# Optimization experiments

Measured on AMD Instinct MI355X. Metric: run time of the kernel, lower is better.

## Reference

```python
import jax, jax.numpy as jnp
import numpy as np

NP = 14      # patches per side
PS = 16      # patch size
L = 12       # transformer blocks
H = 12       # heads
DH = 64      # head dim
D = 768      # hidden dim
S = NP * NP + 1  # 197 tokens
EPS = 1e-5   # torch LayerNorm default eps


def _pos_embed():
    # pos[i, j] = sin(i / 10000^(2*(j//2)/D)) for even j, cos(...) for odd j
    i = jnp.arange(S, dtype=jnp.float32)[:, None]
    j = jnp.arange(D)
    angle = i / jnp.power(jnp.float32(10000.0), (2.0 * (j // 2).astype(jnp.float32)) / D)
    return jnp.where(j % 2 == 0, jnp.sin(angle), jnp.cos(angle))  # [S, D]


def _ln(x, g, b):
    m = jnp.mean(x, axis=-1, keepdims=True)
    v = jnp.mean((x - m) ** 2, axis=-1, keepdims=True)
    return (x - m) / jnp.sqrt(v + EPS) * g + b


def setup_inputs() -> dict:
    key = jax.random.key(0)
    ks = iter(jax.random.split(key, 16))
    r = lambda shape, s=0.02: jax.random.normal(next(ks), shape, dtype=jnp.float32) * s
    return {
        'image': jax.random.normal(next(ks), (32, 3, 224, 224), dtype=jnp.float32),
        'W_embed': r((D, 3 * PS * PS)),
        'b_embed': jnp.zeros((D,), jnp.float32),
        'cls': r((1, D), 1.0),
        'Wq': r((L, H, DH, DH)), 'bq': jnp.zeros((L, H, DH), jnp.float32),
        'Wk': r((L, H, DH, DH)), 'bk': jnp.zeros((L, H, DH), jnp.float32),
        'Wv': r((L, H, DH, DH)), 'bv': jnp.zeros((L, H, DH), jnp.float32),
        'ln1_g': jnp.ones((L, D), jnp.float32), 'ln1_b': jnp.zeros((L, D), jnp.float32),
        'ln2_g': jnp.ones((L, D), jnp.float32), 'ln2_b': jnp.zeros((L, D), jnp.float32),
        'W1': r((L, 4 * D, D)), 'b1': jnp.zeros((L, 4 * D), jnp.float32),
        'W2': r((L, D, 4 * D)), 'b2': jnp.zeros((L, D), jnp.float32),
        'Wh': r((1000, D)), 'bh': jnp.zeros((1000,), jnp.float32),
    }


def reference(image, W_embed, b_embed, cls, Wq, bq, Wk, bk, Wv, bv,
              ln1_g, ln1_b, ln2_g, ln2_b, W1, b1, W2, b2, Wh, bh):
    B = image.shape[0]
    # patchify: (B,C,H,W) -> (B, NP*NP, C*PS*PS), token order row-major over (i,j), flatten order (C,ps,ps)
    patches = image.reshape(B, 3, NP, PS, NP, PS).transpose(0, 2, 4, 1, 3, 5).reshape(B, NP * NP, 3 * PS * PS)
    tokens = patches @ W_embed.T + b_embed                      # [B, 196, D]
    tokens = jnp.concatenate([jnp.broadcast_to(cls[None], (B, 1, D)), tokens], axis=1)  # [B, S, D]
    x = tokens + _pos_embed()[None]
    scale = 1.0 / jnp.sqrt(jnp.float32(DH))
    for l in range(L):
        h = _ln(x, ln1_g[l], ln1_b[l]).reshape(B, S, H, DH)
        q = jnp.einsum('bshd,hed->bshe', h, Wq[l]) + bq[l]
        k = jnp.einsum('bshd,hed->bshe', h, Wk[l]) + bk[l]
        v = jnp.einsum('bshd,hed->bshe', h, Wv[l]) + bv[l]
        att = jax.nn.softmax(jnp.einsum('bshe,bthe->bhst', q, k) * scale, axis=-1)
        o = jnp.einsum('bhst,bthe->bshe', att, v).reshape(B, S, D)
        x = x + o
        h2 = _ln(x, ln2_g[l], ln2_b[l])
        m = jax.nn.gelu(h2 @ W1[l].T + b1[l], approximate=False)  # torch nn.GELU = exact erf
        x = x + m @ W2[l].T + b2[l]
    return x[:, 0] @ Wh.T + bh  # [B, 1000]
```

## Files before the change

### kernel.cpp

```cpp
#include <hip/hip_runtime.h>
#include <math.h>

#define BB 32
#define SS 197
#define DD 768
#define HH 12
#define DHD 64
#define LL 12
#define FF 3072
#define NPATCH 196
#define NTOK (BB * SS)
#define MPAD 6400
#define LNEPS 1e-5f

typedef short bf8_t __attribute__((ext_vector_type(8)));
typedef float f4_t  __attribute__((ext_vector_type(4)));
typedef unsigned short u16x8 __attribute__((ext_vector_type(8)));

__device__ __forceinline__ unsigned short f2bf(float x) {
    unsigned u = __float_as_uint(x);
    return (unsigned short)((u + 0x8000u) >> 16);
}
__device__ __forceinline__ float bf_lo(unsigned u) { return __uint_as_float(u << 16); }

__device__ __forceinline__ void gl_lds16(const void* g, void* l) {
    __builtin_amdgcn_global_load_lds((const __attribute__((address_space(1))) unsigned int*)g,
                                     (__attribute__((address_space(3))) unsigned int*)l, 16, 0, 0);
}

__global__ __launch_bounds__(256) void k_conv(const float* __restrict__ a,
                                              unsigned short* __restrict__ o, int n4) {
    for (int i = blockIdx.x * 256 + threadIdx.x; i < n4; i += gridDim.x * 256) {
        float4 v = ((const float4*)a)[i];
        ushort4 r;
        r.x = f2bf(v.x); r.y = f2bf(v.y); r.z = f2bf(v.z); r.w = f2bf(v.w);
        ((ushort4*)o)[i] = r;
    }
}

__global__ __launch_bounds__(256) void k_patchify(const float* __restrict__ img,
                                                  unsigned short* __restrict__ P) {
    const int total = BB * NPATCH * DD;
    for (int idx = blockIdx.x * 256 + threadIdx.x; idx < total; idx += gridDim.x * 256) {
        int e = idx % DD;
        int rest = idx / DD;
        int p = rest % NPATCH;
        int b = rest / NPATCH;
        int c = e >> 8;
        int pi = (e >> 4) & 15;
        int pj = e & 15;
        int i = p / 14, j = p % 14;
        P[idx] = f2bf(img[(((size_t)b * 3 + c) * 224 + (i * 16 + pi)) * 224 + (j * 16 + pj)]);
    }
}

template <int EPI>
__global__ __launch_bounds__(256) void k_gemm_bf(const unsigned short* __restrict__ A,
                                                 const unsigned short* __restrict__ Bw,
                                                 const float* __restrict__ bias,
                                                 void* __restrict__ Cout,
                                                 int M, int N, int K) {
    __shared__ unsigned short As[128 * 32];
    __shared__ unsigned short Bs[128 * 32];
    const int tid = threadIdx.x;
    const int wave = tid >> 6, lane = tid & 63;
    const int m0 = blockIdx.y << 7, n0 = blockIdx.x << 7;

    const int r0 = tid >> 2, kp = (tid & 3) * 8;
    const unsigned short* gA0 = A + (size_t)(m0 + r0) * K + kp;
    const unsigned short* gA1 = A + (size_t)(m0 + 64 + r0) * K + kp;
    const unsigned short* gB0 = Bw + (size_t)(n0 + r0) * K + kp;
    const unsigned short* gB1 = Bw + (size_t)(n0 + 64 + r0) * K + kp;
    unsigned short* lA0 = &As[tid * 8];
    unsigned short* lA1 = &As[(tid + 256) * 8];
    unsigned short* lB0 = &Bs[tid * 8];
    unsigned short* lB1 = &Bs[(tid + 256) * 8];

    const int mh = (wave >> 1) << 6, nh = (wave & 1) << 6;
    const int lm = lane & 15, kq = lane >> 4;

    f4_t acc[4][4];
#pragma unroll
    for (int i = 0; i < 4; ++i)
#pragma unroll
        for (int j = 0; j < 4; ++j) acc[i][j] = (f4_t){0.f, 0.f, 0.f, 0.f};

    for (int k0 = 0; k0 < K; k0 += 32) {
        gl_lds16(gA0, lA0);
        gl_lds16(gA1, lA1);
        gl_lds16(gB0, lB0);
        gl_lds16(gB1, lB1);
        gA0 += 32; gA1 += 32; gB0 += 32; gB1 += 32;
        __syncthreads();
        bf8_t af[4], bfr[4];
#pragma unroll
        for (int mt = 0; mt < 4; ++mt)
            af[mt] = *(const bf8_t*)&As[(mh + mt * 16 + lm) * 32 + kq * 8];
#pragma unroll
        for (int nt = 0; nt < 4; ++nt)
            bfr[nt] = *(const bf8_t*)&Bs[(nh + nt * 16 + lm) * 32 + kq * 8];
#pragma unroll
        for (int mt = 0; mt < 4; ++mt)
#pragma unroll
            for (int nt = 0; nt < 4; ++nt)
                acc[mt][nt] = __builtin_amdgcn_mfma_f32_16x16x32_bf16(af[mt], bfr[nt],
                                                                      acc[mt][nt], 0, 0, 0);
        __syncthreads();
    }

    const int rbase = m0 + mh + kq * 4;
    const int cbase = n0 + nh + lm;
#pragma unroll
    for (int mt = 0; mt < 4; ++mt) {
#pragma unroll
        for (int nt = 0; nt < 4; ++nt) {
            const int col = cbase + nt * 16;
            const float bv = bias[col];
#pragma unroll
            for (int r = 0; r < 4; ++r) {
                const int row = rbase + mt * 16 + r;
                float val = acc[mt][nt][r] + bv;
                if (EPI == 0) {
                    size_t om = (size_t)(row / 196) * 197 + (row % 196) + 1;
                    ((float*)Cout)[om * DD + col] = val;
                } else if (EPI == 1) {
                    val = 0.5f * val * (1.f + erff(val * 0.7071067811865476f));
                    ((unsigned short*)Cout)[(size_t)row * N + col] = f2bf(val);
                } else {
                    if (row < M) ((float*)Cout)[(size_t)row * DD + col] += val;
                }
            }
        }
    }
}

__global__ __launch_bounds__(256) void k_qkv_mfma(const unsigned short* __restrict__ h,
                                                  const unsigned short* __restrict__ Wqb,
                                                  const unsigned short* __restrict__ Wkb,
                                                  const unsigned short* __restrict__ Wvb,
                                                  const float* __restrict__ bq,
                                                  const float* __restrict__ bk,
                                                  const float* __restrict__ bv,
                                                  unsigned short* __restrict__ qo,
                                                  unsigned short* __restrict__ ko,
                                                  unsigned short* __restrict__ vo) {
    __shared__ unsigned short As[2 * 128 * 32];
    __shared__ unsigned short Bs[3 * 2 * 64 * 32];
    const int head = blockIdx.x;
    const int m0 = blockIdx.y << 7;
    const int tid = threadIdx.x;
    const int wave = tid >> 6, lane = tid & 63;
    const int lm = lane & 15, kq = lane >> 4;

#pragma unroll
    for (int j = 0; j < 4; ++j) {
        int khalf = j >> 1;
        int rem = (j & 1) * 256 + tid;
        int row = rem >> 2, koff = (rem & 3) * 8;
        gl_lds16(h + (size_t)(m0 + row) * DD + head * 64 + khalf * 32 + koff,
                 &As[(j * 256 + tid) * 8]);
    }
    const unsigned short* Wq_h = Wqb + head * 4096;
    const unsigned short* Wk_h = Wkb + head * 4096;
    const unsigned short* Wv_h = Wvb + head * 4096;
#pragma unroll
    for (int j = 0; j < 6; ++j) {
        const unsigned short* src = (j < 2) ? Wq_h : ((j < 4) ? Wk_h : Wv_h);
        int cm = (j & 1) * 256 + tid;
        int khalf = cm >> 8;
        int rem2 = cm & 255;
        int row = rem2 >> 2, koff = (rem2 & 3) * 8;
        gl_lds16(src + row * 64 + khalf * 32 + koff, &Bs[(j * 256 + tid) * 8]);
    }
    __syncthreads();

    f4_t acc[2][12];
#pragma unroll
    for (int i = 0; i < 2; ++i)
#pragma unroll
        for (int j = 0; j < 12; ++j) acc[i][j] = (f4_t){0.f, 0.f, 0.f, 0.f};

#pragma unroll
    for (int kh = 0; kh < 2; ++kh) {
        bf8_t af[2], bfr[12];
#pragma unroll
        for (int mt = 0; mt < 2; ++mt)
            af[mt] = *(const bf8_t*)&As[kh * 4096 + (wave * 32 + mt * 16 + lm) * 32 + kq * 8];
#pragma unroll
        for (int nt = 0; nt < 12; ++nt)
            bfr[nt] = *(const bf8_t*)&Bs[(nt >> 2) * 4096 + kh * 2048 +
                                         ((nt & 3) * 16 + lm) * 32 + kq * 8];
#pragma unroll
        for (int mt = 0; mt < 2; ++mt)
#pragma unroll
            for (int nt = 0; nt < 12; ++nt)
                acc[mt][nt] = __builtin_amdgcn_mfma_f32_16x16x32_bf16(af[mt], bfr[nt],
                                                                      acc[mt][nt], 0, 0, 0);
    }

    const int rbase = m0 + wave * 32 + kq * 4;
#pragma unroll
    for (int mt = 0; mt < 2; ++mt) {
#pragma unroll
        for (int nt = 0; nt < 12; ++nt) {
            const int col = nt * 16 + lm;
            const int e = col & 63;
            const float* bsrc = (nt < 4) ? bq : ((nt < 8) ? bk : bv);
            unsigned short* dst = (nt < 4) ? qo : ((nt < 8) ? ko : vo);
            const float bval = bsrc[head * 64 + e];
#pragma unroll
            for (int r = 0; r < 4; ++r) {
                const int row = rbase + mt * 16 + r;
                if (row < NTOK)
                    dst[(size_t)row * DD + head * 64 + e] = f2bf(acc[mt][nt][r] + bval);
            }
        }
    }
}

__global__ __launch_bounds__(256) void k_posadd(float* __restrict__ x,
                                                const float* __restrict__ cls) {
    const int total = BB * SS * DD;
    const float LN1E4 = 9.210340371976184f;
    for (int idx = blockIdx.x * 256 + threadIdx.x; idx < total; idx += gridDim.x * 256) {
        int d = idx % DD;
        int s = (idx / DD) % SS;
        float ang = (float)s * __expf(-LN1E4 * (float)(2 * (d >> 1)) / 768.f);
        float pv = (d & 1) ? __cosf(ang) : __sinf(ang);
        if (s == 0) x[idx] = cls[d] + pv;
        else        x[idx] += pv;
    }
}

__global__ __launch_bounds__(256) void k_ln2(const float* __restrict__ x,
                                             const float* __restrict__ g,
                                             const float* __restrict__ bp,
                                             unsigned short* __restrict__ out) {
    const int row = blockIdx.x * 4 + (threadIdx.x >> 6);
    const int lane = threadIdx.x & 63;
    if (row >= NTOK) return;
    const float* xr = x + (size_t)row * DD + lane * 12;
    float4 a = ((const float4*)xr)[0];
    float4 b = ((const float4*)xr)[1];
    float4 c = ((const float4*)xr)[2];
    float s = a.x + a.y + a.z + a.w + b.x + b.y + b.z + b.w + c.x + c.y + c.z + c.w;
#pragma unroll
    for (int o = 32; o; o >>= 1) s += __shfl_xor(s, o);
    const float mean = s * (1.f / DD);
    float vr = 0.f, e0;
    e0 = a.x - mean; vr += e0 * e0; e0 = a.y - mean; vr += e0 * e0;
    e0 = a.z - mean; vr += e0 * e0; e0 = a.w - mean; vr += e0 * e0;
    e0 = b.x - mean; vr += e0 * e0; e0 = b.y - mean; vr += e0 * e0;
    e0 = b.z - mean; vr += e0 * e0; e0 = b.w - mean; vr += e0 * e0;
    e0 = c.x - mean; vr += e0 * e0; e0 = c.y - mean; vr += e0 * e0;
    e0 = c.z - mean; vr += e0 * e0; e0 = c.w - mean; vr += e0 * e0;
#pragma unroll
    for (int o = 32; o; o >>= 1) vr += __shfl_xor(vr, o);
    const float rstd = rsqrtf(vr * (1.f / DD) + LNEPS);

    const float4* g4 = (const float4*)(g + lane * 12);
    const float4* b4p = (const float4*)(bp + lane * 12);
    unsigned short* op = out + (size_t)row * DD + lane * 12;
    float4 gv, bv;
    ushort4 r;
    gv = g4[0]; bv = b4p[0];
    r.x = f2bf((a.x - mean) * rstd * gv.x + bv.x);
    r.y = f2bf((a.y - mean) * rstd * gv.y + bv.y);
    r.z = f2bf((a.z - mean) * rstd * gv.z + bv.z);
    r.w = f2bf((a.w - mean) * rstd * gv.w + bv.w);
    ((ushort4*)op)[0] = r;
    gv = g4[1]; bv = b4p[1];
    r.x = f2bf((b.x - mean) * rstd * gv.x + bv.x);
    r.y = f2bf((b.y - mean) * rstd * gv.y + bv.y);
    r.z = f2bf((b.z - mean) * rstd * gv.z + bv.z);
    r.w = f2bf((b.w - mean) * rstd * gv.w + bv.w);
    ((ushort4*)op)[1] = r;
    gv = g4[2]; bv = b4p[2];
    r.x = f2bf((c.x - mean) * rstd * gv.x + bv.x);
    r.y = f2bf((c.y - mean) * rstd * gv.y + bv.y);
    r.z = f2bf((c.z - mean) * rstd * gv.z + bv.z);
    r.w = f2bf((c.w - mean) * rstd * gv.w + bv.w);
    ((ushort4*)op)[2] = r;
}

__global__ __launch_bounds__(256) void k_attn3(const unsigned short* __restrict__ qg,
                                               const unsigned short* __restrict__ kg,
                                               const unsigned short* __restrict__ vg,
                                               float* __restrict__ x) {
    const int qt = blockIdx.x, head = blockIdx.y, b = blockIdx.z;
    const int tid = threadIdx.x, wv = tid >> 6, lane = tid & 63;
    const int lm = lane & 15, kq = lane >> 4;

    __shared__ __align__(16) unsigned short lds[29696];
    unsigned short* Kl = lds;
    unsigned short* Pl = lds;
    unsigned short* Vt = lds + 14848;

    const size_t tokbase = (size_t)b * SS;
    const unsigned short* kb = kg + tokbase * DD + head * 64;
    const unsigned short* vb = vg + tokbase * DD + head * 64;
    const unsigned short* qb = qg + tokbase * DD + head * 64;

#pragma unroll
    for (int it = 0; it < 7; ++it) {
        int c = it * 256 + tid;
        int kh = c / 896, rem = c - kh * 896;
        int t = rem >> 2, cc = rem & 3;
        gl_lds16(kb + (size_t)t * DD + kh * 32 + cc * 8, (char*)lds + c * 16);
    }
#pragma unroll
    for (int it = 0; it < 7; ++it) {
        int idx = it * 256 + tid;
        int t = idx >> 3, eg = idx & 7;
        if (t < SS) {
            u16x8 v8 = *(const u16x8*)(vb + (size_t)t * DD + eg * 8);
#pragma unroll
            for (int j = 0; j < 8; ++j) Vt[(eg * 8 + j) * 232 + t] = v8[j];
        } else {
#pragma unroll
            for (int j = 0; j < 8; ++j) Vt[(eg * 8 + j) * 232 + t] = 0;
        }
    }

    const int qrow = qt * 64 + wv * 16 + lm;
    bf8_t qf0 = *(const bf8_t*)(qb + (size_t)qrow * DD + kq * 8);
    bf8_t qf1 = *(const bf8_t*)(qb + (size_t)qrow * DD + 32 + kq * 8);

    __syncthreads();

    f4_t sacc[13];
#pragma unroll
    for (int tt = 0; tt < 13; ++tt) sacc[tt] = (f4_t){0.f, 0.f, 0.f, 0.f};
#pragma unroll
    for (int tt = 0; tt < 13; ++tt) {
        bf8_t a0 = *(const bf8_t*)&Kl[(tt * 16 + lm) * 32 + kq * 8];
        bf8_t a1 = *(const bf8_t*)&Kl[7168 + (tt * 16 + lm) * 32 + kq * 8];
        sacc[tt] = __builtin_amdgcn_mfma_f32_16x16x32_bf16(a0, qf0, sacc[tt], 0, 0, 0);
        sacc[tt] = __builtin_amdgcn_mfma_f32_16x16x32_bf16(a1, qf1, sacc[tt], 0, 0, 0);
    }

    float mx = -1e30f;
#pragma unroll
    for (int tt = 0; tt < 13; ++tt)
#pragma unroll
        for (int r = 0; r < 4; ++r) {
            float s = sacc[tt][r] * 0.125f;
            if (tt == 12 && (kq * 4 + r) >= 5) s = -1e30f;
            sacc[tt][r] = s;
            mx = fmaxf(mx, s);
        }
    mx = fmaxf(mx, __shfl_xor(mx, 16));
    mx = fmaxf(mx, __shfl_xor(mx, 32));
    float sum = 0.f;
#pragma unroll
    for (int tt = 0; tt < 13; ++tt)
#pragma unroll
        for (int r = 0; r < 4; ++r) {
            float p = __expf(sacc[tt][r] - mx);
            sacc[tt][r] = p;
            sum += p;
        }
    sum += __shfl_xor(sum, 16);
    sum += __shfl_xor(sum, 32);
    const float inv = 1.f / sum;

    __syncthreads();

    unsigned short* Pw = Pl + wv * 3712;
#pragma unroll
    for (int tt = 0; tt < 13; ++tt)
#pragma unroll
        for (int r = 0; r < 4; ++r)
            Pw[lm * 232 + tt * 16 + kq * 4 + r] = f2bf(sacc[tt][r]);
    *(short4*)&Pw[lm * 232 + 208 + kq * 4] = make_short4(0, 0, 0, 0);

    f4_t oacc[4];
#pragma unroll
    for (int et = 0; et < 4; ++et) oacc[et] = (f4_t){0.f, 0.f, 0.f, 0.f};
#pragma unroll
    for (int kc = 0; kc < 7; ++kc) {
        bf8_t pa = *(const bf8_t*)&Pw[lm * 232 + kc * 32 + kq * 8];
#pragma unroll
        for (int et = 0; et < 4; ++et) {
            bf8_t vv = *(const bf8_t*)&Vt[(et * 16 + lm) * 232 + kc * 32 + kq * 8];
            oacc[et] = __builtin_amdgcn_mfma_f32_16x16x32_bf16(pa, vv, oacc[et], 0, 0, 0);
        }
    }

    float invq[4];
#pragma unroll
    for (int r = 0; r < 4; ++r) invq[r] = __shfl(inv, kq * 4 + r);

    float* xp = x + tokbase * DD + head * 64;
#pragma unroll
    for (int r = 0; r < 4; ++r) {
        const int qgr = qt * 64 + wv * 16 + kq * 4 + r;
        if (qgr < SS) {
#pragma unroll
            for (int et = 0; et < 4; ++et)
                xp[(size_t)qgr * DD + et * 16 + lm] += oacc[et][r] * invq[r];
        }
    }
}

__global__ __launch_bounds__(256) void k_head(const float* __restrict__ x,
                                              const float* __restrict__ Wh,
                                              const float* __restrict__ bh,
                                              float* __restrict__ out) {
    const int b = blockIdx.y;
    const int c = blockIdx.x * 256 + threadIdx.x;
    __shared__ __align__(16) float xs[DD];
    const float* xr = x + (size_t)b * SS * DD;
    for (int d = threadIdx.x; d < DD; d += 256) xs[d] = xr[d];
    __syncthreads();
    if (c < 1000) {
        const float4* w4 = (const float4*)(Wh + (size_t)c * DD);
        float acc = 0.f;
#pragma unroll 4
        for (int d4 = 0; d4 < DD / 4; ++d4) {
            float4 w = w4[d4];
            const float4 xv = *(const float4*)&xs[d4 << 2];
            acc += xv.x * w.x + xv.y * w.y + xv.z * w.z + xv.w * w.w;
        }
        out[(size_t)b * 1000 + c] = acc + bh[c];
    }
}

extern "C" void kernel_launch(void* const* d_in, const int* in_sizes, int n_in,
                              void* d_out, int out_size, void* d_ws, size_t ws_size,
                              hipStream_t stream) {
    const float* image   = (const float*)d_in[0];
    const float* W_embed = (const float*)d_in[1];
    const float* b_embed = (const float*)d_in[2];
    const float* cls     = (const float*)d_in[3];
    const float* Wq      = (const float*)d_in[4];
    const float* bq      = (const float*)d_in[5];
    const float* Wk      = (const float*)d_in[6];
    const float* bk      = (const float*)d_in[7];
    const float* Wv      = (const float*)d_in[8];
    const float* bv      = (const float*)d_in[9];
    const float* ln1g    = (const float*)d_in[10];
    const float* ln1b    = (const float*)d_in[11];
    const float* ln2g    = (const float*)d_in[12];
    const float* ln2b    = (const float*)d_in[13];
    const float* W1      = (const float*)d_in[14];
    const float* b1      = (const float*)d_in[15];
    const float* W2      = (const float*)d_in[16];
    const float* b2      = (const float*)d_in[17];
    const float* Wh      = (const float*)d_in[18];
    const float* bh      = (const float*)d_in[19];
    float* out = (float*)d_out;

    float* x = (float*)d_ws;
    unsigned short* h_bf   = (unsigned short*)(x + (size_t)NTOK * DD);
    unsigned short* q_bf   = h_bf + (size_t)MPAD * DD;
    unsigned short* k_bf   = q_bf + (size_t)MPAD * DD;
    unsigned short* v_bf   = k_bf + (size_t)MPAD * DD;
    unsigned short* mlp_bf = v_bf + (size_t)MPAD * DD;
    unsigned short* W1_bf  = mlp_bf + (size_t)MPAD * FF;
    unsigned short* W2_bf  = W1_bf + (size_t)FF * DD;
    unsigned short* We_bf  = W2_bf + (size_t)FF * DD;
    unsigned short* Wq_bf  = We_bf + (size_t)DD * DD;
    unsigned short* Wk_bf  = Wq_bf + (size_t)LL * HH * DHD * DHD;
    unsigned short* Wv_bf  = Wk_bf + (size_t)LL * HH * DHD * DHD;
    unsigned short* P_bf   = mlp_bf;

    const int QKVW = LL * HH * DHD * DHD;

    k_conv<<<576, 256, 0, stream>>>(W_embed, We_bf, DD * DD / 4);
    k_conv<<<576, 256, 0, stream>>>(Wq, Wq_bf, QKVW / 4);
    k_conv<<<576, 256, 0, stream>>>(Wk, Wk_bf, QKVW / 4);
    k_conv<<<576, 256, 0, stream>>>(Wv, Wv_bf, QKVW / 4);

    k_patchify<<<1024, 256, 0, stream>>>(image, P_bf);
    k_gemm_bf<0><<<dim3(6, 49), 256, 0, stream>>>(P_bf, We_bf, b_embed, x,
                                                  BB * NPATCH, DD, DD);
    k_posadd<<<1024, 256, 0, stream>>>(x, cls);

    for (int l = 0; l < LL; ++l) {
        k_ln2<<<(NTOK + 3) / 4, 256, 0, stream>>>(x, ln1g + l * DD, ln1b + l * DD, h_bf);
        k_qkv_mfma<<<dim3(HH, MPAD / 128), 256, 0, stream>>>(
            h_bf, Wq_bf + (size_t)l * HH * 4096, Wk_bf + (size_t)l * HH * 4096,
            Wv_bf + (size_t)l * HH * 4096, bq + l * DD, bk + l * DD, bv + l * DD,
            q_bf, k_bf, v_bf);
        k_attn3<<<dim3(4, HH, BB), 256, 0, stream>>>(q_bf, k_bf, v_bf, x);
        k_ln2<<<(NTOK + 3) / 4, 256, 0, stream>>>(x, ln2g + l * DD, ln2b + l * DD, h_bf);
        k_conv<<<2304, 256, 0, stream>>>(W1 + (size_t)l * FF * DD, W1_bf, FF * DD / 4);
        k_conv<<<2304, 256, 0, stream>>>(W2 + (size_t)l * DD * FF, W2_bf, FF * DD / 4);
        k_gemm_bf<1><<<dim3(FF / 128, MPAD / 128), 256, 0, stream>>>(
            h_bf, W1_bf, b1 + (size_t)l * FF, mlp_bf, NTOK, FF, DD);
        k_gemm_bf<2><<<dim3(DD / 128, MPAD / 128), 256, 0, stream>>>(
            mlp_bf, W2_bf, b2 + (size_t)l * DD, x, NTOK, DD, FF);
    }

    k_head<<<dim3(4, BB), 256, 0, stream>>>(x, Wh, bh, out);
}
```

Before: 3.093 ms.

## Split-K the MLP down-projection with atomic adds and fuse weight conversions

Replaces the second MLP GEMM (K=3072, only 6x50 tiles) with a split-K kernel that uses two K slices and accumulates into the residual stream through atomic float adds. The bias is added only by the first slice. This doubles the block count so the GPU is better occupied. It also merges the two per-layer W1/W2 bf16 conversion launches into one kernel. In exchange it adds atomic traffic and makes the float summation order nondeterministic, and the new GEMM loop is single-buffered.

```diff
diff --git a/kernel.cpp b/kernel.cpp
--- a/kernel.cpp
+++ b/kernel.cpp
@@ -35,6 +35,21 @@
         ushort4 r;
         r.x = f2bf(v.x); r.y = f2bf(v.y); r.z = f2bf(v.z); r.w = f2bf(v.w);
         ((ushort4*)o)[i] = r;
+    }
+}
+
+__global__ __launch_bounds__(256) void k_conv2(const float* __restrict__ a1,
+                                               unsigned short* __restrict__ o1, int n1,
+                                               const float* __restrict__ a2,
+                                               unsigned short* __restrict__ o2, int n2) {
+    for (int i = blockIdx.x * 256 + threadIdx.x; i < n1 + n2; i += gridDim.x * 256) {
+        const float* a = (i < n1) ? a1 : a2;
+        unsigned short* o = (i < n1) ? o1 : o2;
+        int j = (i < n1) ? i : i - n1;
+        float4 v = ((const float4*)a)[j];
+        ushort4 r;
+        r.x = f2bf(v.x); r.y = f2bf(v.y); r.z = f2bf(v.z); r.w = f2bf(v.w);
+        ((ushort4*)o)[j] = r;
     }
 }
 
@@ -129,6 +144,80 @@
                 } else {
                     if (row < M) ((float*)Cout)[(size_t)row * DD + col] += val;
                 }
+            }
+        }
+    }
+}
+
+__global__ __launch_bounds__(256) void k_gemm_sk(const unsigned short* __restrict__ A,
+                                                 const unsigned short* __restrict__ Bw,
+                                                 const float* __restrict__ bias,
+                                                 float* __restrict__ Cout,
+                                                 int M, int N, int K) {
+    __shared__ unsigned short As[128 * 32];
+    __shared__ unsigned short Bs[128 * 32];
+    const int tid = threadIdx.x;
+    const int wave = tid >> 6, lane = tid & 63;
+    const int m0 = blockIdx.y << 7, n0 = blockIdx.x << 7;
+    const int ksplit = K / gridDim.z;
+    const int kbeg = blockIdx.z * ksplit;
+
+    const int r0 = tid >> 2, kp = (tid & 3) * 8;
+    const unsigned short* gA0 = A + (size_t)(m0 + r0) * K + kbeg + kp;
+    const unsigned short* gA1 = A + (size_t)(m0 + 64 + r0) * K + kbeg + kp;
+    const unsigned short* gB0 = Bw + (size_t)(n0 + r0) * K + kbeg + kp;
+    const unsigned short* gB1 = Bw + (size_t)(n0 + 64 + r0) * K + kbeg + kp;
+    unsigned short* lA0 = &As[tid * 8];
+    unsigned short* lA1 = &As[(tid + 256) * 8];
+    unsigned short* lB0 = &Bs[tid * 8];
+    unsigned short* lB1 = &Bs[(tid + 256) * 8];
+
+    const int mh = (wave >> 1) << 6, nh = (wave & 1) << 6;
+    const int lm = lane & 15, kq = lane >> 4;
+
+    f4_t acc[4][4];
+#pragma unroll
+    for (int i = 0; i < 4; ++i)
+#pragma unroll
+        for (int j = 0; j < 4; ++j) acc[i][j] = (f4_t){0.f, 0.f, 0.f, 0.f};
+
+    for (int k0 = 0; k0 < ksplit; k0 += 32) {
+        gl_lds16(gA0, lA0);
+        gl_lds16(gA1, lA1);
+        gl_lds16(gB0, lB0);
+        gl_lds16(gB1, lB1);
+        gA0 += 32; gA1 += 32; gB0 += 32; gB1 += 32;
+        __syncthreads();
+        bf8_t af[4], bfr[4];
+#pragma unroll
+        for (int mt = 0; mt < 4; ++mt)
+            af[mt] = *(const bf8_t*)&As[(mh + mt * 16 + lm) * 32 + kq * 8];
+#pragma unroll
+        for (int nt = 0; nt < 4; ++nt)
+            bfr[nt] = *(const bf8_t*)&Bs[(nh + nt * 16 + lm) * 32 + kq * 8];
+#pragma unroll
+        for (int mt = 0; mt < 4; ++mt)
+#pragma unroll
+            for (int nt = 0; nt < 4; ++nt)
+                acc[mt][nt] = __builtin_amdgcn_mfma_f32_16x16x32_bf16(af[mt], bfr[nt],
+                                                                      acc[mt][nt], 0, 0, 0);
+        __syncthreads();
+    }
+
+    const int rbase = m0 + mh + kq * 4;
+    const int cbase = n0 + nh + lm;
+    const bool addb = (blockIdx.z == 0);
+#pragma unroll
+    for (int mt = 0; mt < 4; ++mt) {
+#pragma unroll
+        for (int nt = 0; nt < 4; ++nt) {
+            const int col = cbase + nt * 16;
+            const float bv = addb ? bias[col] : 0.f;
+#pragma unroll
+            for (int r = 0; r < 4; ++r) {
+                const int row = rbase + mt * 16 + r;
+                if (row < M)
+                    unsafeAtomicAdd(&Cout[(size_t)row * DD + col], acc[mt][nt][r] + bv);
             }
         }
     }
@@ -485,11 +574,11 @@
             q_bf, k_bf, v_bf);
         k_attn3<<<dim3(4, HH, BB), 256, 0, stream>>>(q_bf, k_bf, v_bf, x);
         k_ln2<<<(NTOK + 3) / 4, 256, 0, stream>>>(x, ln2g + l * DD, ln2b + l * DD, h_bf);
-        k_conv<<<2304, 256, 0, stream>>>(W1 + (size_t)l * FF * DD, W1_bf, FF * DD / 4);
-        k_conv<<<2304, 256, 0, stream>>>(W2 + (size_t)l * DD * FF, W2_bf, FF * DD / 4);
+        k_conv2<<<2048, 256, 0, stream>>>(W1 + (size_t)l * FF * DD, W1_bf, FF * DD / 4,
+                                          W2 + (size_t)l * DD * FF, W2_bf, FF * DD / 4);
         k_gemm_bf<1><<<dim3(FF / 128, MPAD / 128), 256, 0, stream>>>(
             h_bf, W1_bf, b1 + (size_t)l * FF, mlp_bf, NTOK, FF, DD);
-        k_gemm_bf<2><<<dim3(DD / 128, MPAD / 128), 256, 0, stream>>>(
+        k_gemm_sk<<<dim3(DD / 128, MPAD / 128, 2), 256, 0, stream>>>(
             mlp_bf, W2_bf, b2 + (size_t)l * DD, x, NTOK, DD, FF);
     }
 
```

Result: faster. 2.935 ms (-5.1%).
